# Performance work log

Hardware: AMD Instinct MI355X
Metric: run time of the kernel (lower is better)

Reference implementation:

```python
import jax, jax.numpy as jnp
import numpy as np

B, T, C, H, E, K = 4, 1024, 1024, 16, 8, 2
HID = 4 * C

def _ln(x, g, b, eps=1e-5):
    m = jnp.mean(x, -1, keepdims=True)
    v = jnp.mean((x - m) ** 2, -1, keepdims=True)
    return (x - m) * jax.lax.rsqrt(v + eps) * g + b

def setup_inputs() -> dict:
    key = jax.random.key(0)
    ks = jax.random.split(key, 8)
    s = 0.02
    return {
        "x": jax.random.normal(ks[0], (B, T, C), jnp.float32),
        "attention_mask": jnp.ones((B, T), jnp.int32),
        "Wq": jax.random.normal(ks[1], (C, C), jnp.float32) * s,
        "bq": jnp.zeros((C,), jnp.float32),
        "Wk": jax.random.normal(ks[2], (C, C), jnp.float32) * s,
        "bk": jnp.zeros((C,), jnp.float32),
        "Wv": jax.random.normal(ks[3], (C, C), jnp.float32) * s,
        "bv": jnp.zeros((C,), jnp.float32),
        "Wo": jax.random.normal(ks[4], (C, C), jnp.float32) * s,
        "bo": jnp.zeros((C,), jnp.float32),
        "ln1_g": jnp.ones((C,), jnp.float32),
        "ln1_b": jnp.zeros((C,), jnp.float32),
        "ln2_g": jnp.ones((C,), jnp.float32),
        "ln2_b": jnp.zeros((C,), jnp.float32),
        "Wr": jax.random.normal(ks[5], (C, E), jnp.float32) * s,
        "br": jnp.zeros((E,), jnp.float32),
        "W1": jax.random.normal(ks[6], (E, C, HID), jnp.float32) * s,
        "b1": jnp.zeros((E, HID), jnp.float32),
        "W2": jax.random.normal(ks[7], (E, HID, C), jnp.float32) * s,
        "b2": jnp.zeros((E, C), jnp.float32),
    }

def reference(x, attention_mask, Wq, bq, Wk, bk, Wv, bv, Wo, bo,
              ln1_g, ln1_b, ln2_g, ln2_b, Wr, br, W1, b1, W2, b2):
    b, t, c = x.shape
    d = c // H
    # --- multi-head self-attention with causal + padding mask ---
    q = (x @ Wq + bq).reshape(b, t, H, d).transpose(0, 2, 1, 3)  # bhtd
    k = (x @ Wk + bk).reshape(b, t, H, d).transpose(0, 2, 1, 3)
    v = (x @ Wv + bv).reshape(b, t, H, d).transpose(0, 2, 1, 3)
    scores = jnp.einsum('bhqd,bhkd->bhqk', q, k) * (1.0 / jnp.sqrt(jnp.float32(d)))
    causal = jnp.tril(jnp.ones((t, t), bool))[None, None]            # [1,1,T,T]
    mask = causal & (attention_mask[:, None, None, :] > 0)          # [B,1,T,T]
    scores = jnp.where(mask, scores, jnp.float32(-1e9))
    attn = jax.nn.softmax(scores, axis=-1)
    o = jnp.einsum('bhqk,bhkd->bhqd', attn, v).transpose(0, 2, 1, 3).reshape(b, t, c)
    mha_out = o @ Wo + bo
    x1 = _ln(x + mha_out, ln1_g, ln1_b)
    # --- sparse MoE: router -> top-k gates -> expert MLPs -> combine ---
    logits = x1 @ Wr + br                               # [B,T,E]
    probs = jax.nn.softmax(logits, axis=-1)
    _, topi = jax.lax.top_k(logits, K)                  # [B,T,K]
    emask = jnp.any(topi[..., None] == jnp.arange(E), axis=-2)  # [B,T,E] bool
    gates = jax.nn.softmax(jnp.where(emask, logits, jnp.float32(-1e9)), axis=-1)
    h = jax.nn.relu(jnp.einsum('btc,ech->bteh', x1, W1) + b1)   # [B,T,E,4C]
    oe = jnp.einsum('bteh,ehc->btec', h, W2) + b2               # [B,T,E,C]
    moe_out = jnp.einsum('btec,bte->btc', oe, gates)
    # load-balancing aux loss: E * sum(mean_prob_e * frac_routed_e)
    importance = probs.mean((0, 1))
    load = emask.astype(probs.dtype).mean((0, 1))
    lb_loss = jnp.float32(E) * jnp.sum(importance * load)
    x2 = _ln(x1 + moe_out, ln2_g, ln2_b)
    return (x2, lb_loss)
```

## Files before the change

kernel.cpp:

```cpp
#include <hip/hip_runtime.h>
#include <hip/hip_bf16.h>

typedef unsigned short u16;
typedef unsigned int u32;
typedef unsigned long long u64;
typedef __attribute__((ext_vector_type(8))) _Float16 half8;
typedef __attribute__((ext_vector_type(8))) short short8;
typedef __attribute__((ext_vector_type(4))) float f32x4;
typedef __attribute__((ext_vector_type(16))) float f32x16;
typedef __attribute__((ext_vector_type(4))) int int4v;

#define DEVI __device__ __forceinline__

static constexpr int TOK = 4096;
static constexpr int CCD = 1024;
static constexpr int HIDD = 4096;
static constexpr int MAXMT = 32;

DEVI u16 f2bf(float f) {
  u32 u = __builtin_bit_cast(u32, f);
  u32 r = (u + 0x7fffu + ((u >> 16) & 1u)) >> 16;
  return (u16)r;
}
DEVI float bf2f(u16 v) { u32 u = ((u32)v) << 16; return __builtin_bit_cast(float, u); }
DEVI u32 pkh2(_Float16 a, _Float16 b) {
  u16 ua = __builtin_bit_cast(u16, a), ub = __builtin_bit_cast(u16, b);
  return (u32)ua | ((u32)ub << 16);
}
union H8U { u32 u[4]; half8 h; };
DEVI f32x16 zero16() { f32x16 z;
#pragma unroll
  for (int i = 0; i < 16; ++i) z[i] = 0.f;
  return z; }
DEVI f32x4 zero4() { f32x4 z;
#pragma unroll
  for (int i = 0; i < 4; ++i) z[i] = 0.f;
  return z; }

DEVI void gload16(const void* g, void* l) {
  __builtin_amdgcn_global_load_lds(
      (const __attribute__((address_space(1))) void*)g,
      (__attribute__((address_space(3))) void*)l, 16, 0, 0);
}

__global__ __launch_bounds__(256) void cast_split_kernel(
    const float* __restrict__ x, _Float16* __restrict__ xh, _Float16* __restrict__ xl) {
  int i = blockIdx.x * 256 + threadIdx.x;
  float4 v = ((const float4*)x)[i];
  _Float16 h0 = (_Float16)v.x, h1 = (_Float16)v.y, h2 = (_Float16)v.z, h3 = (_Float16)v.w;
  _Float16 l0 = (_Float16)(v.x - (float)h0), l1 = (_Float16)(v.y - (float)h1);
  _Float16 l2 = (_Float16)(v.z - (float)h2), l3 = (_Float16)(v.w - (float)h3);
  ((uint2*)xh)[i] = make_uint2(pkh2(h0, h1), pkh2(h2, h3));
  ((uint2*)xl)[i] = make_uint2(pkh2(l0, l1), pkh2(l2, l3));
}

__global__ __launch_bounds__(256) void trans_split_kernel(
    const float* __restrict__ in, _Float16* __restrict__ oh, _Float16* __restrict__ ol,
    int K, int N) {
  __shared__ float tile[32][33];
  int k0 = blockIdx.x * 32, n0 = blockIdx.y * 32;
  int tx = threadIdx.x & 31, ty = threadIdx.x >> 5;
#pragma unroll
  for (int i = 0; i < 4; ++i) { int r = ty + i * 8; tile[r][tx] = in[(size_t)(k0 + r) * N + n0 + tx]; }
  __syncthreads();
#pragma unroll
  for (int i = 0; i < 4; ++i) {
    int r = ty + i * 8;
    float v = tile[tx][r];
    _Float16 h = (_Float16)v;
    oh[(size_t)(n0 + r) * K + k0 + tx] = h;
    ol[(size_t)(n0 + r) * K + k0 + tx] = (_Float16)(v - (float)h);
  }
}

__global__ __launch_bounds__(256) void trans_bf16_kernel(
    const float* __restrict__ in, u16* __restrict__ ob, int K, int N) {
  __shared__ float tile[32][33];
  in += (size_t)blockIdx.z * K * N;
  ob += (size_t)blockIdx.z * K * N;
  int k0 = blockIdx.x * 32, n0 = blockIdx.y * 32;
  int tx = threadIdx.x & 31, ty = threadIdx.x >> 5;
#pragma unroll
  for (int i = 0; i < 4; ++i) { int r = ty + i * 8; tile[r][tx] = in[(size_t)(k0 + r) * N + n0 + tx]; }
  __syncthreads();
#pragma unroll
  for (int i = 0; i < 4; ++i) {
    int r = ty + i * 8;
    ob[(size_t)(n0 + r) * K + k0 + tx] = f2bf(tile[tx][r]);
  }
}

__global__ __launch_bounds__(256) void vtrans_kernel(
    const _Float16* __restrict__ vh, const _Float16* __restrict__ vl,
    _Float16* __restrict__ vth, _Float16* __restrict__ vtl) {
  __shared__ _Float16 t0[32][33], t1[32][33];
  size_t base = (size_t)blockIdx.z * 65536;
  int r0 = blockIdx.x * 32;
  int c0 = blockIdx.y * 32;
  int tx = threadIdx.x & 31, ty = threadIdx.x >> 5;
#pragma unroll
  for (int i = 0; i < 4; ++i) {
    int r = ty + i * 8;
    t0[r][tx] = vh[base + (size_t)(r0 + r) * 64 + c0 + tx];
    t1[r][tx] = vl[base + (size_t)(r0 + r) * 64 + c0 + tx];
  }
  __syncthreads();
#pragma unroll
  for (int i = 0; i < 4; ++i) {
    int r = ty + i * 8;
    vth[base + (size_t)(c0 + r) * 1024 + r0 + tx] = t0[tx][r];
    vtl[base + (size_t)(c0 + r) * 1024 + r0 + tx] = t1[tx][r];
  }
}

template <int EPI>
__global__ __launch_bounds__(512, 4) void gemm_f16x3_kernel(
    const _Float16* __restrict__ Ah, const _Float16* __restrict__ Al,
    const _Float16* __restrict__ Bh, const _Float16* __restrict__ Bl,
    const float* __restrict__ bias0, const float* __restrict__ bias1, const float* __restrict__ bias2,
    _Float16* __restrict__ q_h, _Float16* __restrict__ q_l,
    _Float16* __restrict__ k_h, _Float16* __restrict__ k_l,
    _Float16* __restrict__ v_h, _Float16* __restrict__ v_l,
    float* __restrict__ outf, int M, int N, int K) {
  __shared__ __align__(16) _Float16 sA[2][128 * 64];
  __shared__ __align__(16) _Float16 sB[2][128 * 64];
  const int tid = threadIdx.x;
  const int mt = blockIdx.x, nt = blockIdx.y;
  const int lane = tid & 63, wv = tid >> 6;
  const int wm = wv >> 2, wn = wv & 3;
  f32x4 acc[4][2];
#pragma unroll
  for (int m = 0; m < 4; ++m)
#pragma unroll
    for (int n = 0; n < 2; ++n) acc[m][n] = zero4();

  const _Float16* aS[2]; const _Float16* bS[2];
#pragma unroll
  for (int j = 0; j < 2; ++j) {
    int flat = j * 512 + tid;
    int row = flat >> 3, sg = flat & 7, s = sg ^ (row & 7), g = s >> 1, hl = s & 1;
    aS[j] = (hl ? Al : Ah) + (size_t)(mt * 128 + row) * K + g * 8;
    bS[j] = (hl ? Bl : Bh) + (size_t)(nt * 128 + row) * K + g * 8;
  }

  const int nkt = K >> 5;
#pragma unroll
  for (int j = 0; j < 2; ++j) gload16(aS[j], (char*)sA[0] + (j * 512 + tid) * 16);
#pragma unroll
  for (int j = 0; j < 2; ++j) gload16(bS[j], (char*)sB[0] + (j * 512 + tid) * 16);

  for (int kt = 0; kt < nkt; ++kt) {
    const int cur = kt & 1;
    if (kt + 1 < nkt) {
#pragma unroll
      for (int j = 0; j < 2; ++j) gload16(aS[j] + (kt + 1) * 32, (char*)sA[cur ^ 1] + (j * 512 + tid) * 16);
#pragma unroll
      for (int j = 0; j < 2; ++j) gload16(bS[j] + (kt + 1) * 32, (char*)sB[cur ^ 1] + (j * 512 + tid) * 16);
      asm volatile("s_waitcnt vmcnt(4)" ::: "memory");
    } else {
      asm volatile("s_waitcnt vmcnt(0)" ::: "memory");
    }
    __builtin_amdgcn_s_barrier();
    const int g2 = (lane >> 4) << 1;
    half8 bhf[2], blf[2];
#pragma unroll
    for (int n = 0; n < 2; ++n) {
      int row = wn * 32 + n * 16 + (lane & 15);
      const char* base = (const char*)sB[cur] + row * 128;
      bhf[n] = *(const half8*)(base + (((g2) ^ (row & 7)) << 4));
      blf[n] = *(const half8*)(base + (((g2 + 1) ^ (row & 7)) << 4));
    }
    __builtin_amdgcn_s_setprio(1);
#pragma unroll
    for (int m = 0; m < 4; ++m) {
      int row = wm * 64 + m * 16 + (lane & 15);
      const char* base = (const char*)sA[cur] + row * 128;
      half8 af = *(const half8*)(base + (((g2) ^ (row & 7)) << 4));
      half8 alf = *(const half8*)(base + (((g2 + 1) ^ (row & 7)) << 4));
#pragma unroll
      for (int n = 0; n < 2; ++n) {
        acc[m][n] = __builtin_amdgcn_mfma_f32_16x16x32_f16(af, bhf[n], acc[m][n], 0, 0, 0);
        acc[m][n] = __builtin_amdgcn_mfma_f32_16x16x32_f16(af, blf[n], acc[m][n], 0, 0, 0);
        acc[m][n] = __builtin_amdgcn_mfma_f32_16x16x32_f16(alf, bhf[n], acc[m][n], 0, 0, 0);
      }
    }
    __builtin_amdgcn_s_setprio(0);
    __builtin_amdgcn_s_barrier();
  }
#pragma unroll
  for (int m = 0; m < 4; ++m) {
    int lrow = wm * 64 + m * 16 + ((lane >> 4) << 2);
#pragma unroll
    for (int n = 0; n < 2; ++n) {
      int gcol = nt * 128 + wn * 32 + n * 16 + (lane & 15);
      f32x4 a = acc[m][n];
#pragma unroll
      for (int j = 0; j < 4; ++j) {
        int grow = mt * 128 + lrow + j;
        float v = a[j];
        if (EPI == 0) {
          int sec = gcol >> 10, cc = gcol & 1023;
          v += (sec == 0 ? bias0[cc] : (sec == 1 ? bias1[cc] : bias2[cc]));
          int hh = cc >> 6, dd = cc & 63;
          int bb = grow >> 10, tt = grow & 1023;
          size_t dst = (((size_t)(bb * 16 + hh)) * 1024 + tt) * 64 + dd;
          _Float16 hi = (_Float16)v;
          _Float16 lo = (_Float16)(v - (float)hi);
          if (sec == 0) { q_h[dst] = hi; q_l[dst] = lo; }
          else if (sec == 1) { k_h[dst] = hi; k_l[dst] = lo; }
          else { v_h[dst] = hi; v_l[dst] = lo; }
        } else {
          v += bias0[gcol];
          outf[(size_t)grow * N + gcol] = v;
        }
      }
    }
  }
}

__global__ __launch_bounds__(256) void attn_kernel(
    const _Float16* __restrict__ qhp, const _Float16* __restrict__ qlp,
    const _Float16* __restrict__ khp, const _Float16* __restrict__ klp,
    const _Float16* __restrict__ vth, const _Float16* __restrict__ vtl,
    const int* __restrict__ amask,
    _Float16* __restrict__ ohp, _Float16* __restrict__ olp) {
  const int lane = threadIdx.x & 63;
  const int wv = threadIdx.x >> 6;
  const int bh = blockIdx.x >> 3;
  const int qblk = (blockIdx.x & 7) + wv * 8;
  const int b = bh >> 4, hh = bh & 15;
  const int q0 = qblk * 32;
  const int qln = lane & 31;
  const int qq = q0 + qln;
  const int hf = lane >> 5;
  __shared__ float lmadd[1024];
  for (int i = threadIdx.x; i < 1024; i += 256) lmadd[i] = (amask[b * 1024 + i] > 0) ? 0.f : -1e9f;
  __syncthreads();

  size_t qoff = ((size_t)bh * 1024 + qq) * 64 + hf * 8;
  half8 qfh[4], qfl[4];
#pragma unroll
  for (int d = 0; d < 4; ++d) {
    qfh[d] = *(const half8*)(qhp + qoff + d * 16);
    qfl[d] = *(const half8*)(qlp + qoff + d * 16);
  }
  f32x16 o0 = zero16(), o1 = zero16();
  float mrun = -3.0e38f, lsum = 0.f;
  const float LOG2E = 1.44269504088896f;

  for (int kb = 0; kb <= qblk; ++kb) {
    size_t koff = ((size_t)bh * 1024 + kb * 32 + qln) * 64 + hf * 8;
    f32x16 s = zero16();
#pragma unroll
    for (int d = 0; d < 4; ++d) {
      half8 kfh = *(const half8*)(khp + koff + d * 16);
      half8 kfl = *(const half8*)(klp + koff + d * 16);
      s = __builtin_amdgcn_mfma_f32_32x32x16_f16(kfh, qfh[d], s, 0, 0, 0);
      s = __builtin_amdgcn_mfma_f32_32x32x16_f16(kfh, qfl[d], s, 0, 0, 0);
      s = __builtin_amdgcn_mfma_f32_32x32x16_f16(kfl, qfh[d], s, 0, 0, 0);
    }
    float sc[16];
#pragma unroll
    for (int r = 0; r < 16; ++r) {
      int krow = (r & 3) + ((r >> 2) << 3) + (hf << 2);
      int key = kb * 32 + krow;
      sc[r] = s[r] * 0.125f + lmadd[key];
    }
    if (kb == qblk) {
#pragma unroll
      for (int r = 0; r < 16; ++r) {
        int krow = (r & 3) + ((r >> 2) << 3) + (hf << 2);
        if (kb * 32 + krow > qq) sc[r] = -1e9f;
      }
    }
    float pm = sc[0];
#pragma unroll
    for (int r = 1; r < 16; ++r) pm = fmaxf(pm, sc[r]);
    pm = fmaxf(pm, __shfl_xor(pm, 32));
    float mnew = fmaxf(mrun, pm);
    float aold = exp2f((mrun - mnew) * LOG2E);
    float p[16]; float psum = 0.f;
#pragma unroll
    for (int r = 0; r < 16; ++r) { p[r] = exp2f((sc[r] - mnew) * LOG2E); psum += p[r]; }
    lsum = lsum * aold + psum;
#pragma unroll
    for (int j = 0; j < 16; ++j) { o0[j] *= aold; o1[j] *= aold; }
    mrun = mnew;
    u32 hd[8], ld[8];
#pragma unroll
    for (int i = 0; i < 8; ++i) {
      _Float16 h0 = (_Float16)p[2 * i], h1 = (_Float16)p[2 * i + 1];
      hd[i] = pkh2(h0, h1);
      ld[i] = pkh2((_Float16)(p[2 * i] - (float)h0), (_Float16)(p[2 * i + 1] - (float)h1));
    }
    auto mkfrag = [&](u32 d0, u32 d1, u32 d2, u32 d3) -> half8 {
      u32 e0 = (u32)__shfl_xor((int)d0, 32);
      u32 e1 = (u32)__shfl_xor((int)d1, 32);
      u32 e2 = (u32)__shfl_xor((int)d2, 32);
      u32 e3 = (u32)__shfl_xor((int)d3, 32);
      H8U t;
      t.u[0] = hf ? e2 : d0;
      t.u[1] = hf ? e3 : d1;
      t.u[2] = hf ? d2 : e0;
      t.u[3] = hf ? d3 : e1;
      return t.h;
    };
    half8 pbh0 = mkfrag(hd[0], hd[1], hd[2], hd[3]);
    half8 pbl0 = mkfrag(ld[0], ld[1], ld[2], ld[3]);
    half8 pbh1 = mkfrag(hd[4], hd[5], hd[6], hd[7]);
    half8 pbl1 = mkfrag(ld[4], ld[5], ld[6], ld[7]);
    size_t vb = ((size_t)bh * 64 + qln) * 1024 + kb * 32 + hf * 8;
    half8 vh00 = *(const half8*)(vth + vb);
    half8 vh01 = *(const half8*)(vth + vb + 16);
    half8 vh10 = *(const half8*)(vth + vb + 32 * 1024);
    half8 vh11 = *(const half8*)(vth + vb + 32 * 1024 + 16);
    half8 vl00 = *(const half8*)(vtl + vb);
    half8 vl01 = *(const half8*)(vtl + vb + 16);
    half8 vl10 = *(const half8*)(vtl + vb + 32 * 1024);
    half8 vl11 = *(const half8*)(vtl + vb + 32 * 1024 + 16);
    o0 = __builtin_amdgcn_mfma_f32_32x32x16_f16(vh00, pbh0, o0, 0, 0, 0);
    o0 = __builtin_amdgcn_mfma_f32_32x32x16_f16(vh00, pbl0, o0, 0, 0, 0);
    o0 = __builtin_amdgcn_mfma_f32_32x32x16_f16(vl00, pbh0, o0, 0, 0, 0);
    o0 = __builtin_amdgcn_mfma_f32_32x32x16_f16(vh01, pbh1, o0, 0, 0, 0);
    o0 = __builtin_amdgcn_mfma_f32_32x32x16_f16(vh01, pbl1, o0, 0, 0, 0);
    o0 = __builtin_amdgcn_mfma_f32_32x32x16_f16(vl01, pbh1, o0, 0, 0, 0);
    o1 = __builtin_amdgcn_mfma_f32_32x32x16_f16(vh10, pbh0, o1, 0, 0, 0);
    o1 = __builtin_amdgcn_mfma_f32_32x32x16_f16(vh10, pbl0, o1, 0, 0, 0);
    o1 = __builtin_amdgcn_mfma_f32_32x32x16_f16(vl10, pbh0, o1, 0, 0, 0);
    o1 = __builtin_amdgcn_mfma_f32_32x32x16_f16(vh11, pbh1, o1, 0, 0, 0);
    o1 = __builtin_amdgcn_mfma_f32_32x32x16_f16(vh11, pbl1, o1, 0, 0, 0);
    o1 = __builtin_amdgcn_mfma_f32_32x32x16_f16(vl11, pbh1, o1, 0, 0, 0);
  }
  lsum += __shfl_xor(lsum, 32);
  float inv = 1.f / lsum;
  size_t obase = ((size_t)(b * 1024 + qq)) * 1024 + hh * 64;
#pragma unroll
  for (int dt = 0; dt < 2; ++dt) {
#pragma unroll
    for (int c = 0; c < 4; ++c) {
      int dloc = dt * 32 + c * 8 + hf * 4;
      float v0, v1, v2, v3;
      if (dt == 0) { v0 = o0[4 * c] * inv; v1 = o0[4 * c + 1] * inv; v2 = o0[4 * c + 2] * inv; v3 = o0[4 * c + 3] * inv; }
      else { v0 = o1[4 * c] * inv; v1 = o1[4 * c + 1] * inv; v2 = o1[4 * c + 2] * inv; v3 = o1[4 * c + 3] * inv; }
      _Float16 h0 = (_Float16)v0, h1 = (_Float16)v1, h2 = (_Float16)v2, h3 = (_Float16)v3;
      *(uint2*)(ohp + obase + dloc) = make_uint2(pkh2(h0, h1), pkh2(h2, h3));
      *(uint2*)(olp + obase + dloc) = make_uint2(
          pkh2((_Float16)(v0 - (float)h0), (_Float16)(v1 - (float)h1)),
          pkh2((_Float16)(v2 - (float)h2), (_Float16)(v3 - (float)h3)));
    }
  }
}

__global__ __launch_bounds__(256) void ln1_kernel(
    const float* __restrict__ x, const float* __restrict__ mha,
    const float* __restrict__ gam, const float* __restrict__ bet,
    float* __restrict__ x1f, u16* __restrict__ x1b) {
  int t = blockIdx.x, tid = threadIdx.x;
  const float* xr = x + (size_t)t * 1024;
  const float* mr = mha + (size_t)t * 1024;
  float v[4], s = 0.f, ss = 0.f;
#pragma unroll
  for (int i = 0; i < 4; ++i) { int c = tid + i * 256; float a = xr[c] + mr[c]; v[i] = a; s += a; ss += a * a; }
#pragma unroll
  for (int o = 32; o; o >>= 1) { s += __shfl_xor(s, o); ss += __shfl_xor(ss, o); }
  __shared__ float rs[4], rss[4];
  int wv = tid >> 6;
  if ((tid & 63) == 0) { rs[wv] = s; rss[wv] = ss; }
  __syncthreads();
  s = rs[0] + rs[1] + rs[2] + rs[3];
  ss = rss[0] + rss[1] + rss[2] + rss[3];
  float mean = s * (1.f / 1024.f);
  float var = ss * (1.f / 1024.f) - mean * mean;
  float rstd = rsqrtf(var + 1e-5f);
#pragma unroll
  for (int i = 0; i < 4; ++i) {
    int c = tid + i * 256;
    float y = (v[i] - mean) * rstd * gam[c] + bet[c];
    x1f[(size_t)t * 1024 + c] = y;
    x1b[(size_t)t * 1024 + c] = f2bf(y);
  }
}

__global__ __launch_bounds__(256) void router_kernel(
    const float* __restrict__ x1f, const float* __restrict__ Wr, const float* __restrict__ br,
    int* __restrict__ eids, float* __restrict__ gatesv, float* __restrict__ probbuf) {
  int wv = threadIdx.x >> 6, lane = threadIdx.x & 63;
  int t = blockIdx.x * 4 + wv;
  const float* xr = x1f + (size_t)t * 1024;
  float acc[8];
#pragma unroll
  for (int e = 0; e < 8; ++e) acc[e] = 0.f;
  for (int c = lane; c < 1024; c += 64) {
    float xv = xr[c];
    const float* wr = Wr + c * 8;
#pragma unroll
    for (int e = 0; e < 8; ++e) acc[e] += xv * wr[e];
  }
#pragma unroll
  for (int e = 0; e < 8; ++e) {
#pragma unroll
    for (int o = 32; o; o >>= 1) acc[e] += __shfl_xor(acc[e], o);
    acc[e] += br[e];
  }
  if (lane == 0) {
    float mx = acc[0];
#pragma unroll
    for (int e = 1; e < 8; ++e) mx = fmaxf(mx, acc[e]);
    float pe[8], se = 0.f;
#pragma unroll
    for (int e = 0; e < 8; ++e) { pe[e] = expf(acc[e] - mx); se += pe[e]; }
    float inv = 1.f / se;
#pragma unroll
    for (int e = 0; e < 8; ++e) probbuf[(size_t)t * 8 + e] = pe[e] * inv;
    int i0 = 0;
#pragma unroll
    for (int e = 1; e < 8; ++e) if (acc[e] > acc[i0]) i0 = e;
    int i1 = -1;
#pragma unroll
    for (int e = 0; e < 8; ++e) if (e != i0 && (i1 < 0 || acc[e] > acc[i1])) i1 = e;
    float m2 = fmaxf(acc[i0], acc[i1]);
    float g0 = expf(acc[i0] - m2), g1 = expf(acc[i1] - m2);
    float gs = 1.f / (g0 + g1);
    eids[t * 2] = i0; eids[t * 2 + 1] = i1;
    gatesv[t * 2] = g0 * gs; gatesv[t * 2 + 1] = g1 * gs;
  }
}

__global__ __launch_bounds__(256) void count_offs_kernel(
    const int* __restrict__ eids, int* __restrict__ counts, int* __restrict__ offs) {
  __shared__ int lc[8];
  if (threadIdx.x < 8) lc[threadIdx.x] = 0;
  __syncthreads();
  for (int i = threadIdx.x; i < TOK * 2; i += 256) atomicAdd(&lc[eids[i]], 1);
  __syncthreads();
  if (threadIdx.x == 0) {
    int s = 0;
#pragma unroll
    for (int e = 0; e < 8; ++e) { counts[e] = lc[e]; offs[e] = s; s += lc[e]; }
    offs[8] = s;
  }
}

__global__ __launch_bounds__(256) void scatter_kernel(
    const int* __restrict__ eids, const int* __restrict__ offs, int* __restrict__ cursor,
    int* __restrict__ tlist, int* __restrict__ invx) {
  int t = blockIdx.x * 256 + threadIdx.x;
  int lane = threadIdx.x & 63;
#pragma unroll
  for (int s = 0; s < 2; ++s) {
    int e = eids[t * 2 + s];
#pragma unroll
    for (int ex = 0; ex < 8; ++ex) {
      u64 m = __ballot(e == ex);
      if (e == ex) {
        int leader = __ffsll((long long)m) - 1;
        int rank = __popcll(m & ((1ull << lane) - 1ull));
        int base = 0;
        if (lane == leader) base = atomicAdd(&cursor[ex], __popcll(m));
        base = __shfl(base, leader);
        int idx = offs[ex] + base + rank;
        tlist[idx] = t;
        invx[t * 2 + s] = idx;
      }
    }
  }
}

template <int EPI>
__global__ __launch_bounds__(512, 4) void gemm_bf16_kernel(
    const u16* __restrict__ Abase, const u16* __restrict__ Bbase, const float* __restrict__ bias,
    u16* __restrict__ outb, float* __restrict__ outf,
    const int* __restrict__ tlist, const int* __restrict__ offs,
    int K, int ldA, int N, int NTILES) {
  int bid = blockIdx.x;
  int e = bid / (MAXMT * NTILES);
  int rem = bid % (MAXMT * NTILES);
  int mt = rem / NTILES, nt = rem % NTILES;
  int mstart = offs[e], mend = offs[e + 1];
  int ne = mend - mstart;
  if (mt * 128 >= ne) return;
  const int half = blockIdx.y;
  const int kOff = half * K;
  const u16* Bt = Bbase + (size_t)e * N * ldA;
  const float* bvec = bias + (size_t)e * N;
  __shared__ __align__(16) u16 sA[3][128 * 32];
  __shared__ __align__(16) u16 sB[3][128 * 32];
  const int tid = threadIdx.x;
  const int lane = tid & 63, wv = tid >> 6;
  const int wm = wv >> 2, wn = wv & 3;
  f32x4 acc[4][2];
#pragma unroll
  for (int m = 0; m < 4; ++m)
#pragma unroll
    for (int n = 0; n < 2; ++n) acc[m][n] = zero4();

  const int row = tid >> 2, sg = tid & 3, g = sg ^ (row & 3);
  int rl = mt * 128 + row;
  if (rl >= ne) rl = ne - 1;
  size_t arow = (EPI == 2) ? (size_t)tlist[mstart + rl] : (size_t)(mstart + rl);
  const u16* aS = Abase + arow * ldA + kOff + g * 8;
  const u16* bS = Bt + (size_t)(nt * 128 + row) * ldA + kOff + g * 8;

  const int nkt = K >> 5;
  gload16(aS, (char*)sA[0] + tid * 16);
  gload16(bS, (char*)sB[0] + tid * 16);
  gload16(aS + 32, (char*)sA[1] + tid * 16);
  gload16(bS + 32, (char*)sB[1] + tid * 16);

  int slot = 0;
  for (int kt = 0; kt < nkt; ++kt) {
    if (kt + 2 < nkt) {
      int ps = slot + 2; if (ps >= 3) ps -= 3;
      gload16(aS + (kt + 2) * 32, (char*)sA[ps] + tid * 16);
      gload16(bS + (kt + 2) * 32, (char*)sB[ps] + tid * 16);
    }
    int remt = nkt - 1 - kt;
    if (remt >= 2) asm volatile("s_waitcnt vmcnt(4)" ::: "memory");
    else if (remt == 1) asm volatile("s_waitcnt vmcnt(2)" ::: "memory");
    else asm volatile("s_waitcnt vmcnt(0)" ::: "memory");
    __builtin_amdgcn_s_barrier();
    const int gg = lane >> 4;
    short8 bfr[2];
#pragma unroll
    for (int n = 0; n < 2; ++n) {
      int r2 = wn * 32 + n * 16 + (lane & 15);
      bfr[n] = *(const short8*)((const char*)sB[slot] + r2 * 64 + ((gg ^ (r2 & 3)) << 4));
    }
    __builtin_amdgcn_s_setprio(1);
#pragma unroll
    for (int m = 0; m < 4; ++m) {
      int ra = wm * 64 + m * 16 + (lane & 15);
      short8 afr = *(const short8*)((const char*)sA[slot] + ra * 64 + ((gg ^ (ra & 3)) << 4));
#pragma unroll
      for (int n = 0; n < 2; ++n)
        acc[m][n] = __builtin_amdgcn_mfma_f32_16x16x32_bf16(afr, bfr[n], acc[m][n], 0, 0, 0);
    }
    __builtin_amdgcn_s_setprio(0);
    __builtin_amdgcn_s_barrier();
    ++slot; if (slot == 3) slot = 0;
  }
#pragma unroll
  for (int m = 0; m < 4; ++m) {
    int lrow = wm * 64 + m * 16 + ((lane >> 4) << 2);
#pragma unroll
    for (int n = 0; n < 2; ++n) {
      int col = nt * 128 + wn * 32 + n * 16 + (lane & 15);
      f32x4 a = acc[m][n];
#pragma unroll
      for (int j = 0; j < 4; ++j) {
        int rl2 = mt * 128 + lrow + j;
        if (rl2 < ne) {
          size_t pair = (size_t)(mstart + rl2);
          float v = a[j] + ((EPI == 2 || half == 0) ? bvec[col] : 0.f);
          if (EPI == 2) { v = fmaxf(v, 0.f); outb[pair * N + col] = f2bf(v); }
          else outb[((size_t)half * 8192 + pair) * N + col] = f2bf(v);
        }
      }
    }
  }
}

__global__ __launch_bounds__(256) void ln2_kernel(
    const float* __restrict__ x1f, const u16* __restrict__ oe,
    const int* __restrict__ invx, const float* __restrict__ gatesv,
    const float* __restrict__ gam, const float* __restrict__ bet, float* __restrict__ out) {
  int t = blockIdx.x, tid = threadIdx.x;
  int i0 = invx[t * 2], i1 = invx[t * 2 + 1];
  float g0 = gatesv[t * 2], g1 = gatesv[t * 2 + 1];
  const u16* r0a = oe + (size_t)i0 * 1024;
  const u16* r0b = oe + (size_t)(8192 + i0) * 1024;
  const u16* r1a = oe + (size_t)i1 * 1024;
  const u16* r1b = oe + (size_t)(8192 + i1) * 1024;
  const float* xr = x1f + (size_t)t * 1024;
  float v[4], s = 0.f, ss = 0.f;
#pragma unroll
  for (int i = 0; i < 4; ++i) {
    int c = tid + i * 256;
    float a = xr[c] + g0 * (bf2f(r0a[c]) + bf2f(r0b[c])) + g1 * (bf2f(r1a[c]) + bf2f(r1b[c]));
    v[i] = a; s += a; ss += a * a;
  }
#pragma unroll
  for (int o = 32; o; o >>= 1) { s += __shfl_xor(s, o); ss += __shfl_xor(ss, o); }
  __shared__ float rs[4], rss[4];
  int wv = tid >> 6;
  if ((tid & 63) == 0) { rs[wv] = s; rss[wv] = ss; }
  __syncthreads();
  s = rs[0] + rs[1] + rs[2] + rs[3];
  ss = rss[0] + rss[1] + rss[2] + rss[3];
  float mean = s * (1.f / 1024.f);
  float var = ss * (1.f / 1024.f) - mean * mean;
  float rstd = rsqrtf(var + 1e-5f);
#pragma unroll
  for (int i = 0; i < 4; ++i) {
    int c = tid + i * 256;
    out[(size_t)t * 1024 + c] = (v[i] - mean) * rstd * gam[c] + bet[c];
  }
}

__global__ __launch_bounds__(256) void loss_kernel(
    const float* __restrict__ probbuf, const int* __restrict__ counts,
    float* __restrict__ out) {
  __shared__ float ps[256][8];
  float a[8];
#pragma unroll
  for (int e = 0; e < 8; ++e) a[e] = 0.f;
  for (int r = threadIdx.x; r < TOK; r += 256) {
#pragma unroll
    for (int e = 0; e < 8; ++e) a[e] += probbuf[(size_t)r * 8 + e];
  }
#pragma unroll
  for (int e = 0; e < 8; ++e) ps[threadIdx.x][e] = a[e];
  __syncthreads();
  if (threadIdx.x == 0) {
    float s = 0.f;
#pragma unroll
    for (int e = 0; e < 8; ++e) {
      float imp = 0.f;
      for (int i = 0; i < 256; ++i) imp += ps[i][e];
      s += (imp * (1.f / 4096.f)) * ((float)counts[e] * (1.f / 4096.f));
    }
    out[0] = 8.f * s;
  }
}

extern "C" void kernel_launch(void* const* d_in, const int* in_sizes, int n_in,
                              void* d_out, int out_size, void* d_ws, size_t ws_size,
                              hipStream_t stream) {
  const float* x = (const float*)d_in[0];
  const int* amask = (const int*)d_in[1];
  const float* Wq = (const float*)d_in[2]; const float* bq = (const float*)d_in[3];
  const float* Wk = (const float*)d_in[4]; const float* bk = (const float*)d_in[5];
  const float* Wv = (const float*)d_in[6]; const float* bv = (const float*)d_in[7];
  const float* Wo = (const float*)d_in[8]; const float* bo = (const float*)d_in[9];
  const float* g1 = (const float*)d_in[10]; const float* be1 = (const float*)d_in[11];
  const float* g2 = (const float*)d_in[12]; const float* be2 = (const float*)d_in[13];
  const float* Wr = (const float*)d_in[14]; const float* br = (const float*)d_in[15];
  const float* W1 = (const float*)d_in[16]; const float* b1 = (const float*)d_in[17];
  const float* W2 = (const float*)d_in[18]; const float* b2 = (const float*)d_in[19];
  float* out = (float*)d_out;

  char* w = (char*)d_ws;
  auto alloc = [&](size_t bytes) -> char* {
    char* p = w; w += (bytes + 255) & ~(size_t)255; return p;
  };
  _Float16* xsh = (_Float16*)alloc((size_t)TOK * CCD * 2);
  _Float16* xsl = (_Float16*)alloc((size_t)TOK * CCD * 2);
  _Float16* wqh = (_Float16*)alloc((size_t)3072 * 1024 * 2);
  _Float16* wql = (_Float16*)alloc((size_t)3072 * 1024 * 2);
  _Float16* woh = (_Float16*)alloc((size_t)1024 * 1024 * 2);
  _Float16* wol = (_Float16*)alloc((size_t)1024 * 1024 * 2);
  _Float16* qhi = (_Float16*)alloc((size_t)TOK * CCD * 2);
  _Float16* qlo = (_Float16*)alloc((size_t)TOK * CCD * 2);
  _Float16* khi = (_Float16*)alloc((size_t)TOK * CCD * 2);
  _Float16* klo = (_Float16*)alloc((size_t)TOK * CCD * 2);
  _Float16* vhi = (_Float16*)alloc((size_t)TOK * CCD * 2);
  _Float16* vlo = (_Float16*)alloc((size_t)TOK * CCD * 2);
  _Float16* vthi = (_Float16*)alloc((size_t)TOK * CCD * 2);
  _Float16* vtlo = (_Float16*)alloc((size_t)TOK * CCD * 2);
  _Float16* ohi = (_Float16*)alloc((size_t)TOK * CCD * 2);
  _Float16* olo = (_Float16*)alloc((size_t)TOK * CCD * 2);
  float* mha = (float*)alloc((size_t)TOK * CCD * 4);
  float* x1f = (float*)alloc((size_t)TOK * CCD * 4);
  u16* x1b = (u16*)alloc((size_t)TOK * CCD * 2);
  u16* w1t = (u16*)alloc((size_t)8 * HIDD * CCD * 2);
  u16* w2t = (u16*)alloc((size_t)8 * CCD * HIDD * 2);
  u16* hbuf = (u16*)alloc((size_t)8192 * HIDD * 2);
  float* probbuf = (float*)alloc((size_t)TOK * 8 * 4);
  int* eids = (int*)alloc(TOK * 2 * 4);
  float* gatesv = (float*)alloc(TOK * 2 * 4);
  int* invx = (int*)alloc(TOK * 2 * 4);
  int* tlist = (int*)alloc(8192 * 4);
  char* ctrl = alloc(4096);
  int* counts = (int*)ctrl;
  int* cursor = counts + 8;
  int* offs = counts + 16;
  u16* oe = (u16*)qhi;

  hipMemsetAsync(ctrl, 0, 256, stream);

  cast_split_kernel<<<4096, 256, 0, stream>>>(x, xsh, xsl);
  trans_split_kernel<<<dim3(32, 32), 256, 0, stream>>>(Wq, wqh, wql, 1024, 1024);
  trans_split_kernel<<<dim3(32, 32), 256, 0, stream>>>(Wk, wqh + (size_t)1024 * 1024, wql + (size_t)1024 * 1024, 1024, 1024);
  trans_split_kernel<<<dim3(32, 32), 256, 0, stream>>>(Wv, wqh + (size_t)2048 * 1024, wql + (size_t)2048 * 1024, 1024, 1024);
  trans_split_kernel<<<dim3(32, 32), 256, 0, stream>>>(Wo, woh, wol, 1024, 1024);
  trans_bf16_kernel<<<dim3(32, 128, 8), 256, 0, stream>>>(W1, w1t, 1024, 4096);
  trans_bf16_kernel<<<dim3(128, 32, 8), 256, 0, stream>>>(W2, w2t, 4096, 1024);

  gemm_f16x3_kernel<0><<<dim3(32, 24), 512, 0, stream>>>(
      xsh, xsl, wqh, wql, bq, bk, bv,
      qhi, qlo, khi, klo, vhi, vlo, nullptr, 4096, 3072, 1024);
  vtrans_kernel<<<dim3(32, 2, 64), 256, 0, stream>>>(vhi, vlo, vthi, vtlo);
  attn_kernel<<<512, 256, 0, stream>>>(qhi, qlo, khi, klo, vthi, vtlo, amask, ohi, olo);
  gemm_f16x3_kernel<1><<<dim3(32, 8), 512, 0, stream>>>(
      ohi, olo, woh, wol, bo, nullptr, nullptr,
      nullptr, nullptr, nullptr, nullptr, nullptr, nullptr, mha, 4096, 1024, 1024);
  ln1_kernel<<<4096, 256, 0, stream>>>(x, mha, g1, be1, x1f, x1b);
  router_kernel<<<1024, 256, 0, stream>>>(x1f, Wr, br, eids, gatesv, probbuf);
  count_offs_kernel<<<1, 256, 0, stream>>>(eids, counts, offs);
  scatter_kernel<<<16, 256, 0, stream>>>(eids, offs, cursor, tlist, invx);
  gemm_bf16_kernel<2><<<dim3(8 * MAXMT * 32, 1), 512, 0, stream>>>(
      x1b, w1t, b1, hbuf, nullptr, tlist, offs, 1024, 1024, 4096, 32);
  gemm_bf16_kernel<3><<<dim3(8 * MAXMT * 8, 2), 512, 0, stream>>>(
      hbuf, w2t, b2, oe, nullptr, nullptr, offs, 2048, 4096, 1024, 8);
  ln2_kernel<<<4096, 256, 0, stream>>>(x1f, oe, invx, gatesv, g2, be2, out);
  loss_kernel<<<1, 256, 0, stream>>>(probbuf, counts, out + (size_t)TOK * CCD);
}
```

Before: 699.2 us.

## Use 256-thread blocks with 64x64 warp tiles in expert GEMM

Restructures the MoE expert bf16 GEMM from 8 waves each computing a 64x32 sub-tile to 4 waves each computing 64x64, keeping the 128x128 block tile. A and B tiles are merged into one interleaved shared buffer with an 8-way XOR swizzle, and each thread now issues four 16-byte global-to-LDS loads per stage. The aim is more MFMAs per LDS fragment read and fewer waves contending for barriers. The cost is more accumulator registers per thread and fewer waves per block to hide latency.

```diff
diff --git a/kernel.cpp b/kernel.cpp
--- a/kernel.cpp
+++ b/kernel.cpp
@@ -467,7 +467,7 @@
 }
 
 template <int EPI>
-__global__ __launch_bounds__(512, 4) void gemm_bf16_kernel(
+__global__ __launch_bounds__(256, 3) void gemm_bf16_kernel(
     const u16* __restrict__ Abase, const u16* __restrict__ Bbase, const float* __restrict__ bias,
     u16* __restrict__ outb, float* __restrict__ outf,
     const int* __restrict__ tlist, const int* __restrict__ offs,
@@ -483,56 +483,65 @@
   const int kOff = half * K;
   const u16* Bt = Bbase + (size_t)e * N * ldA;
   const float* bvec = bias + (size_t)e * N;
-  __shared__ __align__(16) u16 sA[3][128 * 32];
-  __shared__ __align__(16) u16 sB[3][128 * 32];
+  __shared__ __align__(16) u16 sAB[3][128 * 64];
   const int tid = threadIdx.x;
   const int lane = tid & 63, wv = tid >> 6;
-  const int wm = wv >> 2, wn = wv & 3;
-  f32x4 acc[4][2];
+  const int wm = wv >> 1, wn = wv & 1;
+  f32x4 acc[4][4];
 #pragma unroll
   for (int m = 0; m < 4; ++m)
 #pragma unroll
-    for (int n = 0; n < 2; ++n) acc[m][n] = zero4();
-
-  const int row = tid >> 2, sg = tid & 3, g = sg ^ (row & 3);
-  int rl = mt * 128 + row;
-  if (rl >= ne) rl = ne - 1;
-  size_t arow = (EPI == 2) ? (size_t)tlist[mstart + rl] : (size_t)(mstart + rl);
-  const u16* aS = Abase + arow * ldA + kOff + g * 8;
-  const u16* bS = Bt + (size_t)(nt * 128 + row) * ldA + kOff + g * 8;
+    for (int n = 0; n < 4; ++n) acc[m][n] = zero4();
+
+  const u16* src[4];
+#pragma unroll
+  for (int j = 0; j < 4; ++j) {
+    int flat = j * 256 + tid;
+    int r = flat >> 3, sg = flat & 7, v = sg ^ (r & 7);
+    int mat = v >> 2, ch = v & 3;
+    if (mat == 0) {
+      int rl = mt * 128 + r;
+      if (rl >= ne) rl = ne - 1;
+      size_t arow = (EPI == 2) ? (size_t)tlist[mstart + rl] : (size_t)(mstart + rl);
+      src[j] = Abase + arow * ldA + kOff + ch * 8;
+    } else {
+      src[j] = Bt + (size_t)(nt * 128 + r) * ldA + kOff + ch * 8;
+    }
+  }
 
   const int nkt = K >> 5;
-  gload16(aS, (char*)sA[0] + tid * 16);
-  gload16(bS, (char*)sB[0] + tid * 16);
-  gload16(aS + 32, (char*)sA[1] + tid * 16);
-  gload16(bS + 32, (char*)sB[1] + tid * 16);
+#pragma unroll
+  for (int j = 0; j < 4; ++j) gload16(src[j], (char*)sAB[0] + (j * 256 + tid) * 16);
+#pragma unroll
+  for (int j = 0; j < 4; ++j) gload16(src[j] + 32, (char*)sAB[1] + (j * 256 + tid) * 16);
 
   int slot = 0;
   for (int kt = 0; kt < nkt; ++kt) {
     if (kt + 2 < nkt) {
       int ps = slot + 2; if (ps >= 3) ps -= 3;
-      gload16(aS + (kt + 2) * 32, (char*)sA[ps] + tid * 16);
-      gload16(bS + (kt + 2) * 32, (char*)sB[ps] + tid * 16);
+#pragma unroll
+      for (int j = 0; j < 4; ++j) gload16(src[j] + (kt + 2) * 32, (char*)sAB[ps] + (j * 256 + tid) * 16);
     }
     int remt = nkt - 1 - kt;
-    if (remt >= 2) asm volatile("s_waitcnt vmcnt(4)" ::: "memory");
-    else if (remt == 1) asm volatile("s_waitcnt vmcnt(2)" ::: "memory");
+    if (remt >= 2) asm volatile("s_waitcnt vmcnt(8)" ::: "memory");
+    else if (remt == 1) asm volatile("s_waitcnt vmcnt(4)" ::: "memory");
     else asm volatile("s_waitcnt vmcnt(0)" ::: "memory");
     __builtin_amdgcn_s_barrier();
     const int gg = lane >> 4;
-    short8 bfr[2];
-#pragma unroll
-    for (int n = 0; n < 2; ++n) {
-      int r2 = wn * 32 + n * 16 + (lane & 15);
-      bfr[n] = *(const short8*)((const char*)sB[slot] + r2 * 64 + ((gg ^ (r2 & 3)) << 4));
+    const char* base = (const char*)sAB[slot];
+    short8 bfr[4];
+#pragma unroll
+    for (int n = 0; n < 4; ++n) {
+      int R = wn * 64 + n * 16 + (lane & 15);
+      bfr[n] = *(const short8*)(base + R * 128 + (((4 | gg) ^ (R & 7)) << 4));
     }
     __builtin_amdgcn_s_setprio(1);
 #pragma unroll
     for (int m = 0; m < 4; ++m) {
-      int ra = wm * 64 + m * 16 + (lane & 15);
-      short8 afr = *(const short8*)((const char*)sA[slot] + ra * 64 + ((gg ^ (ra & 3)) << 4));
-#pragma unroll
-      for (int n = 0; n < 2; ++n)
+      int R = wm * 64 + m * 16 + (lane & 15);
+      short8 afr = *(const short8*)(base + R * 128 + ((gg ^ (R & 7)) << 4));
+#pragma unroll
+      for (int n = 0; n < 4; ++n)
         acc[m][n] = __builtin_amdgcn_mfma_f32_16x16x32_bf16(afr, bfr[n], acc[m][n], 0, 0, 0);
     }
     __builtin_amdgcn_s_setprio(0);
@@ -543,8 +552,8 @@
   for (int m = 0; m < 4; ++m) {
     int lrow = wm * 64 + m * 16 + ((lane >> 4) << 2);
 #pragma unroll
-    for (int n = 0; n < 2; ++n) {
-      int col = nt * 128 + wn * 32 + n * 16 + (lane & 15);
+    for (int n = 0; n < 4; ++n) {
+      int col = nt * 128 + wn * 64 + n * 16 + (lane & 15);
       f32x4 a = acc[m][n];
 #pragma unroll
       for (int j = 0; j < 4; ++j) {
@@ -698,9 +707,9 @@
   router_kernel<<<1024, 256, 0, stream>>>(x1f, Wr, br, eids, gatesv, probbuf);
   count_offs_kernel<<<1, 256, 0, stream>>>(eids, counts, offs);
   scatter_kernel<<<16, 256, 0, stream>>>(eids, offs, cursor, tlist, invx);
-  gemm_bf16_kernel<2><<<dim3(8 * MAXMT * 32, 1), 512, 0, stream>>>(
+  gemm_bf16_kernel<2><<<dim3(8 * MAXMT * 32, 1), 256, 0, stream>>>(
       x1b, w1t, b1, hbuf, nullptr, tlist, offs, 1024, 1024, 4096, 32);
-  gemm_bf16_kernel<3><<<dim3(8 * MAXMT * 8, 2), 512, 0, stream>>>(
+  gemm_bf16_kernel<3><<<dim3(8 * MAXMT * 8, 2), 256, 0, stream>>>(
       hbuf, w2t, b2, oe, nullptr, nullptr, offs, 2048, 4096, 1024, 8);
   ln2_kernel<<<4096, 256, 0, stream>>>(x1f, oe, invx, gatesv, g2, be2, out);
   loss_kernel<<<1, 256, 0, stream>>>(probbuf, counts, out + (size_t)TOK * CCD);
```

Measured after the change: 706.3 us. Within noise of the previous version (+1.0%).
